# Optimization experiments

Measured on AMD Instinct MI355X. Metric: run time of the kernel, lower is better.

## Reference

```python
import jax, jax.numpy as jnp
import numpy as np

B, L, N_INP, N_HID = 128, 1000, 1, 1024
DT = 0.042
RHO = 0.99
INPUT_SCALING = 1.0
THETA_LIF = 1.0
THETA_RF = 1.0
LIF_TAU_M = 20.0
TAU_REF = 0.25
CONNECTIVITY = 0.1
GAMMA_RANGE = (2.7, 2.9)
EPS_RANGE = (4.7, 4.9)


def setup_inputs() -> dict:
    key = jax.random.key(0)
    x = jax.random.normal(key, (B, L, N_INP), dtype=jnp.float32)
    rng = np.random.default_rng(0)
    # per-unit oscillator params (tuple branch of __init__)
    gamma = rng.uniform(GAMMA_RANGE[0], GAMMA_RANGE[1], N_HID).astype(np.float32)
    epsilon = rng.uniform(EPS_RANGE[0], EPS_RANGE[1], N_HID).astype(np.float32)
    # recurrent matrix: uniform in [-2,2], rescaled to spectral norm rho
    h2h = rng.uniform(-2.0, 2.0, (N_HID, N_HID)).astype(np.float32)
    h2h = h2h * (RHO / np.linalg.norm(h2h, 2)).astype(np.float32)
    x2h = (rng.uniform(0.0, 1.0, (N_INP, N_HID)) * INPUT_SCALING).astype(np.float32)
    bias = ((rng.uniform(0.0, 1.0, N_HID) * 2.0 - 1.0) * INPUT_SCALING).astype(np.float32)
    mask = (rng.uniform(size=(N_HID, N_HID)) < CONNECTIVITY).astype(np.float32)
    lif2hrf = ((rng.uniform(0.0, 1.0, (N_HID, N_HID)) * 2.0 - 1.0) * 2.0 * mask).astype(np.float32)
    return {
        "x": x,
        "x2h": jnp.asarray(x2h),
        "h2h": jnp.asarray(h2h),
        "bias": jnp.asarray(bias),
        "lif2hrf": jnp.asarray(lif2hrf),
        "gamma": jnp.asarray(gamma),
        "epsilon": jnp.asarray(epsilon),
    }


def reference(x, x2h, h2h, bias, lif2hrf, gamma, epsilon):
    dtype = x.dtype
    Bv, Lv, _ = x.shape
    ref_decay = jnp.exp(jnp.asarray(-DT / TAU_REF, dtype))

    def step(carry, xt):
        hy, hz, lif_v, s, ref_p, hy_sum, hy_sq, hrf_n, lif_n = carry
        # input current: (B,I)@(I,H) + (B,H)@(H,H) + (H,)
        cur = xt @ x2h + s @ h2h + bias
        lif_v = lif_v + DT * (-lif_v / LIF_TAU_M + cur)
        lif_s = (lif_v > THETA_LIF).astype(dtype)
        lif_v = lif_v - lif_s * THETA_LIF
        drive = lif_s @ lif2hrf
        hz = hz + DT * (drive - gamma * hy - epsilon * hz)
        hy = hy + DT * hz
        s_new = (hy - THETA_RF - ref_p > 0).astype(dtype)
        # alpha = beta = 0 in bio_cell -> hy, hz unchanged by reset
        ref_p = ref_p * ref_decay + s_new
        hy_sum = hy_sum + hy
        hy_sq = hy_sq + hy * hy
        hrf_n = hrf_n + s_new.sum()
        lif_n = lif_n + lif_s.sum()
        return (hy, hz, lif_v, s_new, ref_p, hy_sum, hy_sq, hrf_n, lif_n), None

    z = jnp.zeros((Bv, N_HID), dtype)
    carry0 = (z, z, z, z, z, z, z, jnp.zeros((), dtype), jnp.zeros((), dtype))
    xs = jnp.swapaxes(x, 0, 1)  # (L, B, I)
    (hy, hz, lif_v, s, ref_p, hy_sum, hy_sq, hrf_n, lif_n), _ = jax.lax.scan(step, carry0, xs)

    hy_mean = hy_sum / Lv
    hy_rms = jnp.sqrt(hy_sq / Lv + 1e-8)
    hy_std = jnp.sqrt(jnp.clip(hy_sq / Lv - hy_mean ** 2, 1e-8))
    features = jnp.concatenate([hy_rms, hy_std, hy], axis=1)  # (B, 3*H)
    denom = Bv * Lv * N_HID
    r_hrf = hrf_n / denom
    r_lif = lif_n / denom
    r_total = r_hrf  # count_lif_spikes=False
    return features, r_total, r_hrf, r_lif
```

## Files before the change

kernel.cpp:

```cpp
#include <hip/hip_runtime.h>

#define NHID    1024
#define BATCH   128
#define LSTEPS  1000
#define DTC     0.042f
#define THETA   1.0f
#define TAUM    20.0f
#define LISTCAP 1032

__global__ __launch_bounds__(1024) void coesn_sim(
    const float* __restrict__ x,
    const float* __restrict__ x2h,
    const float* __restrict__ h2h,
    const float* __restrict__ bias,
    const float* __restrict__ lif2hrf,
    const float* __restrict__ gamma_,
    const float* __restrict__ eps_,
    float* __restrict__ out,
    unsigned int* __restrict__ ws)
{
    const int b    = blockIdx.x;
    const int h    = threadIdx.x;
    const int wv   = h >> 6;
    const int lane = h & 63;

    __shared__ unsigned int Ls[LISTCAP];
    __shared__ unsigned int Ll[LISTCAP];
    __shared__ int Cs[16], Cl[16];
    __shared__ unsigned int red[16];

    Ls[h] = 0; Ll[h] = 0;
    if (h < LISTCAP - 1024) { Ls[1024 + h] = 0; Ll[1024 + h] = 0; }
    if (h < 16) { Cs[h] = 0; Cl[h] = 0; }

    float hy = 0.f, hz = 0.f, v = 0.f, rp = 0.f;
    float hysum = 0.f, hysq = 0.f;
    unsigned int chrf = 0, clif = 0;

    const float g    = gamma_[h];
    const float e    = eps_[h];
    const float bi   = bias[h];
    const float win  = x2h[h];
    const float ref_decay = expf((float)(-0.042 / 0.25));
    const float* xb  = x + (size_t)b * LSTEPS;

    const char* hb = (const char*)h2h     + 4 * (size_t)h;
    const char* lb = (const char*)lif2hrf + 4 * (size_t)h;

    const unsigned long long below = (1ULL << lane) - 1ULL;

    int ns = 0;

    __syncthreads();

    for (int t = 0; t < LSTEPS; ++t) {
        const float xv = xb[t];
        float cur = xv * win + bi;
        for (int k = 0; k < ns; k += 8) {
            const unsigned o0 = Ls[k+0], o1 = Ls[k+1], o2 = Ls[k+2], o3 = Ls[k+3];
            const unsigned o4 = Ls[k+4], o5 = Ls[k+5], o6 = Ls[k+6], o7 = Ls[k+7];
            const float a0 = *(const float*)(hb + o0);
            const float a1 = *(const float*)(hb + o1);
            const float a2 = *(const float*)(hb + o2);
            const float a3 = *(const float*)(hb + o3);
            const float a4 = *(const float*)(hb + o4);
            const float a5 = *(const float*)(hb + o5);
            const float a6 = *(const float*)(hb + o6);
            const float a7 = *(const float*)(hb + o7);
            cur += a0;
            cur += (k+1 < ns) ? a1 : 0.0f;
            cur += (k+2 < ns) ? a2 : 0.0f;
            cur += (k+3 < ns) ? a3 : 0.0f;
            cur += (k+4 < ns) ? a4 : 0.0f;
            cur += (k+5 < ns) ? a5 : 0.0f;
            cur += (k+6 < ns) ? a6 : 0.0f;
            cur += (k+7 < ns) ? a7 : 0.0f;
        }

        v = v + DTC * (-v / TAUM + cur);
        const float lsp = (v > THETA) ? 1.f : 0.f;
        v -= lsp * THETA;
        clif += (unsigned)lsp;
        const unsigned long long balL = __ballot(lsp > 0.5f);
        if (lane == 0) Cl[wv] = __popcll(balL);
        __syncthreads();
        int pre = 0, nl = 0;
        for (int i = 0; i < 16; ++i) { const int c = Cl[i]; pre += (i < wv) ? c : 0; nl += c; }
        if (lsp > 0.5f) Ll[pre + __popcll(balL & below)] = (unsigned)(h * 4096);
        __syncthreads();

        float dr = 0.f;
        for (int k = 0; k < nl; k += 8) {
            const unsigned o0 = Ll[k+0], o1 = Ll[k+1], o2 = Ll[k+2], o3 = Ll[k+3];
            const unsigned o4 = Ll[k+4], o5 = Ll[k+5], o6 = Ll[k+6], o7 = Ll[k+7];
            const float a0 = *(const float*)(lb + o0);
            const float a1 = *(const float*)(lb + o1);
            const float a2 = *(const float*)(lb + o2);
            const float a3 = *(const float*)(lb + o3);
            const float a4 = *(const float*)(lb + o4);
            const float a5 = *(const float*)(lb + o5);
            const float a6 = *(const float*)(lb + o6);
            const float a7 = *(const float*)(lb + o7);
            dr += a0;
            dr += (k+1 < nl) ? a1 : 0.0f;
            dr += (k+2 < nl) ? a2 : 0.0f;
            dr += (k+3 < nl) ? a3 : 0.0f;
            dr += (k+4 < nl) ? a4 : 0.0f;
            dr += (k+5 < nl) ? a5 : 0.0f;
            dr += (k+6 < nl) ? a6 : 0.0f;
            dr += (k+7 < nl) ? a7 : 0.0f;
        }

        hz = hz + DTC * (dr - g * hy - e * hz);
        hy = hy + DTC * hz;
        const float sn = ((hy - THETA - rp) > 0.f) ? 1.f : 0.f;
        rp = rp * ref_decay + sn;
        hysum += hy;
        hysq  += hy * hy;
        chrf += (unsigned)sn;
        const unsigned long long balS = __ballot(sn > 0.5f);
        if (lane == 0) Cs[wv] = __popcll(balS);
        __syncthreads();
        pre = 0; ns = 0;
        for (int i = 0; i < 16; ++i) { const int c = Cs[i]; pre += (i < wv) ? c : 0; ns += c; }
        if (sn > 0.5f) Ls[pre + __popcll(balS & below)] = (unsigned)(h * 4096);
        __syncthreads();
    }

    const float Lf   = (float)LSTEPS;
    const float mean = hysum / Lf;
    const float rms  = sqrtf(hysq / Lf + 1e-8f);
    float var = hysq / Lf - mean * mean;
    var = fmaxf(var, 1e-8f);
    float* ob = out + (size_t)b * (3 * NHID);
    ob[h]            = rms;
    ob[NHID + h]     = sqrtf(var);
    ob[2 * NHID + h] = hy;

    unsigned int c = chrf;
    for (int off = 32; off > 0; off >>= 1) c += __shfl_down(c, off, 64);
    if (lane == 0) red[wv] = c;
    __syncthreads();
    if (h == 0) {
        unsigned int tot = 0;
        for (int i = 0; i < 16; ++i) tot += red[i];
        ws[b * 2] = tot;
    }
    __syncthreads();
    c = clif;
    for (int off = 32; off > 0; off >>= 1) c += __shfl_down(c, off, 64);
    if (lane == 0) red[wv] = c;
    __syncthreads();
    if (h == 0) {
        unsigned int tot = 0;
        for (int i = 0; i < 16; ++i) tot += red[i];
        ws[b * 2 + 1] = tot;
    }
}

__global__ void coesn_final(const unsigned int* __restrict__ ws,
                            float* __restrict__ out)
{
    if (threadIdx.x == 0 && blockIdx.x == 0) {
        unsigned long long hrf = 0, lif = 0;
        for (int b = 0; b < BATCH; ++b) {
            hrf += ws[b * 2];
            lif += ws[b * 2 + 1];
        }
        const float denom = (float)BATCH * (float)LSTEPS * (float)NHID;
        const float r_hrf = (float)hrf / denom;
        const float r_lif = (float)lif / denom;
        float* s = out + (size_t)BATCH * 3 * NHID;
        s[0] = r_hrf;
        s[1] = r_hrf;
        s[2] = r_lif;
    }
}

extern "C" void kernel_launch(void* const* d_in, const int* in_sizes, int n_in,
                              void* d_out, int out_size, void* d_ws, size_t ws_size,
                              hipStream_t stream) {
    const float* x       = (const float*)d_in[0];
    const float* x2h     = (const float*)d_in[1];
    const float* h2h     = (const float*)d_in[2];
    const float* bias    = (const float*)d_in[3];
    const float* lif2hrf = (const float*)d_in[4];
    const float* gamma_  = (const float*)d_in[5];
    const float* eps_    = (const float*)d_in[6];
    float* out = (float*)d_out;
    unsigned int* wsp = (unsigned int*)d_ws;

    coesn_sim<<<BATCH, NHID, 0, stream>>>(x, x2h, h2h, bias, lif2hrf, gamma_, eps_, out, wsp);
    coesn_final<<<1, 64, 0, stream>>>(wsp, out);
}
```

Measured before the change: 1.584 ms.

## Broadcast spike lists via readlane and software-pipeline sparse row gathers

Each wave now loads the first 256 spike-list entries from LDS into registers (one per lane) and uses readlane to turn each offset into a scalar. This replaces per-iteration LDS loads of list indices and makes row addresses wave-uniform. The gather loop is software-pipelined so the next 8 rows load while the previous 8 are accumulated. The wave-count prefix sum also switches from 16 LDS reads to one LDS read plus readlane broadcasts. Lists longer than 256 entries fall back to a slow scalar tail loop, and the padded list capacity is removed.

```diff
diff --git a/kernel.cpp b/kernel.cpp
--- a/kernel.cpp
+++ b/kernel.cpp
@@ -6,7 +6,53 @@
 #define DTC     0.042f
 #define THETA   1.0f
 #define TAUM    20.0f
-#define LISTCAP 1032
+
+#define RL(VS,I)  ((unsigned)__builtin_amdgcn_readlane((VS),(I)))
+
+__device__ __forceinline__ float gather_rows(float acc, const char* mat, int h,
+                                             const unsigned* __restrict__ Lds,
+                                             int v0, int v1, int v2, int v3, int n)
+{
+    if (n <= 0) return acc;
+    const int nf = (n < 256) ? n : 256;
+    const int M  = (nf + 7) & ~7;
+    float c0,c1,c2,c3,c4,c5,c6,c7;
+    {
+        const unsigned q0=RL(v0,0),q1=RL(v0,1),q2=RL(v0,2),q3=RL(v0,3),
+                       q4=RL(v0,4),q5=RL(v0,5),q6=RL(v0,6),q7=RL(v0,7);
+        c0=((const float*)(mat+q0))[h]; c1=((const float*)(mat+q1))[h];
+        c2=((const float*)(mat+q2))[h]; c3=((const float*)(mat+q3))[h];
+        c4=((const float*)(mat+q4))[h]; c5=((const float*)(mat+q5))[h];
+        c6=((const float*)(mat+q6))[h]; c7=((const float*)(mat+q7))[h];
+    }
+    int k = 8;
+    #pragma unroll 1
+    for (; k < M; k += 8) {
+        const int vs = (k < 64) ? v0 : (k < 128) ? v1 : (k < 192) ? v2 : v3;
+        const int kb = k & 63;
+        const unsigned t0=RL(vs,kb+0),t1=RL(vs,kb+1),t2=RL(vs,kb+2),t3=RL(vs,kb+3),
+                       t4=RL(vs,kb+4),t5=RL(vs,kb+5),t6=RL(vs,kb+6),t7=RL(vs,kb+7);
+        const float d0=((const float*)(mat+t0))[h], d1=((const float*)(mat+t1))[h],
+                    d2=((const float*)(mat+t2))[h], d3=((const float*)(mat+t3))[h],
+                    d4=((const float*)(mat+t4))[h], d5=((const float*)(mat+t5))[h],
+                    d6=((const float*)(mat+t6))[h], d7=((const float*)(mat+t7))[h];
+        acc += c0; acc += c1; acc += c2; acc += c3;
+        acc += c4; acc += c5; acc += c6; acc += c7;
+        c0=d0; c1=d1; c2=d2; c3=d3; c4=d4; c5=d5; c6=d6; c7=d7;
+    }
+    const int base = k - 8;
+    acc += c0;
+    acc += (base+1 < nf) ? c1 : 0.0f;
+    acc += (base+2 < nf) ? c2 : 0.0f;
+    acc += (base+3 < nf) ? c3 : 0.0f;
+    acc += (base+4 < nf) ? c4 : 0.0f;
+    acc += (base+5 < nf) ? c5 : 0.0f;
+    acc += (base+6 < nf) ? c6 : 0.0f;
+    acc += (base+7 < nf) ? c7 : 0.0f;
+    for (int kk = 256; kk < n; ++kk)
+        acc += ((const float*)(mat + Lds[kk]))[h];
+    return acc;
+}
 
 __global__ __launch_bounds__(1024) void coesn_sim(
     const float* __restrict__ x,
@@ -23,14 +69,14 @@
     const int h    = threadIdx.x;
     const int wv   = h >> 6;
     const int lane = h & 63;
-
-    __shared__ unsigned int Ls[LISTCAP];
-    __shared__ unsigned int Ll[LISTCAP];
+    const int wvs  = __builtin_amdgcn_readfirstlane(wv);
+
+    __shared__ unsigned int Ls[1024];
+    __shared__ unsigned int Ll[1024];
     __shared__ int Cs[16], Cl[16];
     __shared__ unsigned int red[16];
 
     Ls[h] = 0; Ll[h] = 0;
-    if (h < LISTCAP - 1024) { Ls[1024 + h] = 0; Ll[1024 + h] = 0; }
     if (h < 16) { Cs[h] = 0; Cl[h] = 0; }
 
     float hy = 0.f, hz = 0.f, v = 0.f, rp = 0.f;
@@ -44,8 +90,8 @@
     const float ref_decay = expf((float)(-0.042 / 0.25));
     const float* xb  = x + (size_t)b * LSTEPS;
 
-    const char* hb = (const char*)h2h     + 4 * (size_t)h;
-    const char* lb = (const char*)lif2hrf + 4 * (size_t)h;
+    const char* hmat = (const char*)h2h;
+    const char* lmat = (const char*)lif2hrf;
 
     const unsigned long long below = (1ULL << lane) - 1ULL;
 
@@ -54,62 +100,36 @@
     __syncthreads();
 
     for (int t = 0; t < LSTEPS; ++t) {
+        const int s0 = (int)Ls[lane];
+        const int s1 = (int)Ls[64 + lane];
+        const int s2 = (int)Ls[128 + lane];
+        const int s3 = (int)Ls[192 + lane];
         const float xv = xb[t];
-        float cur = xv * win + bi;
-        for (int k = 0; k < ns; k += 8) {
-            const unsigned o0 = Ls[k+0], o1 = Ls[k+1], o2 = Ls[k+2], o3 = Ls[k+3];
-            const unsigned o4 = Ls[k+4], o5 = Ls[k+5], o6 = Ls[k+6], o7 = Ls[k+7];
-            const float a0 = *(const float*)(hb + o0);
-            const float a1 = *(const float*)(hb + o1);
-            const float a2 = *(const float*)(hb + o2);
-            const float a3 = *(const float*)(hb + o3);
-            const float a4 = *(const float*)(hb + o4);
-            const float a5 = *(const float*)(hb + o5);
-            const float a6 = *(const float*)(hb + o6);
-            const float a7 = *(const float*)(hb + o7);
-            cur += a0;
-            cur += (k+1 < ns) ? a1 : 0.0f;
-            cur += (k+2 < ns) ? a2 : 0.0f;
-            cur += (k+3 < ns) ? a3 : 0.0f;
-            cur += (k+4 < ns) ? a4 : 0.0f;
-            cur += (k+5 < ns) ? a5 : 0.0f;
-            cur += (k+6 < ns) ? a6 : 0.0f;
-            cur += (k+7 < ns) ? a7 : 0.0f;
-        }
+        const float cur = gather_rows(xv * win + bi, hmat, h, Ls, s0, s1, s2, s3, ns);
 
         v = v + DTC * (-v / TAUM + cur);
         const float lsp = (v > THETA) ? 1.f : 0.f;
         v -= lsp * THETA;
         clif += (unsigned)lsp;
         const unsigned long long balL = __ballot(lsp > 0.5f);
-        if (lane == 0) Cl[wv] = __popcll(balL);
-        __syncthreads();
+        if (lane == 0) Cl[wv] = (int)__popcll(balL);
+        __syncthreads();
+        int cv = Cl[lane & 15];
         int pre = 0, nl = 0;
-        for (int i = 0; i < 16; ++i) { const int c = Cl[i]; pre += (i < wv) ? c : 0; nl += c; }
-        if (lsp > 0.5f) Ll[pre + __popcll(balL & below)] = (unsigned)(h * 4096);
-        __syncthreads();
-
-        float dr = 0.f;
-        for (int k = 0; k < nl; k += 8) {
-            const unsigned o0 = Ll[k+0], o1 = Ll[k+1], o2 = Ll[k+2], o3 = Ll[k+3];
-            const unsigned o4 = Ll[k+4], o5 = Ll[k+5], o6 = Ll[k+6], o7 = Ll[k+7];
-            const float a0 = *(const float*)(lb + o0);
-            const float a1 = *(const float*)(lb + o1);
-            const float a2 = *(const float*)(lb + o2);
-            const float a3 = *(const float*)(lb + o3);
-            const float a4 = *(const float*)(lb + o4);
-            const float a5 = *(const float*)(lb + o5);
-            const float a6 = *(const float*)(lb + o6);
-            const float a7 = *(const float*)(lb + o7);
-            dr += a0;
-            dr += (k+1 < nl) ? a1 : 0.0f;
-            dr += (k+2 < nl) ? a2 : 0.0f;
-            dr += (k+3 < nl) ? a3 : 0.0f;
-            dr += (k+4 < nl) ? a4 : 0.0f;
-            dr += (k+5 < nl) ? a5 : 0.0f;
-            dr += (k+6 < nl) ? a6 : 0.0f;
-            dr += (k+7 < nl) ? a7 : 0.0f;
+        #pragma unroll
+        for (int i = 0; i < 16; ++i) {
+            const int ci = __builtin_amdgcn_readlane(cv, i);
+            nl += ci;
+            pre += (i < wvs) ? ci : 0;
         }
+        if (lsp > 0.5f) Ll[pre + (int)__popcll(balL & below)] = (unsigned)(h * 4096);
+        __syncthreads();
+
+        const int l0 = (int)Ll[lane];
+        const int l1 = (int)Ll[64 + lane];
+        const int l2 = (int)Ll[128 + lane];
+        const int l3 = (int)Ll[192 + lane];
+        const float dr = gather_rows(0.0f, lmat, h, Ll, l0, l1, l2, l3, nl);
 
         hz = hz + DTC * (dr - g * hy - e * hz);
         hy = hy + DTC * hz;
@@ -119,11 +139,17 @@
         hysq  += hy * hy;
         chrf += (unsigned)sn;
         const unsigned long long balS = __ballot(sn > 0.5f);
-        if (lane == 0) Cs[wv] = __popcll(balS);
-        __syncthreads();
+        if (lane == 0) Cs[wv] = (int)__popcll(balS);
+        __syncthreads();
+        cv = Cs[lane & 15];
         pre = 0; ns = 0;
-        for (int i = 0; i < 16; ++i) { const int c = Cs[i]; pre += (i < wv) ? c : 0; ns += c; }
-        if (sn > 0.5f) Ls[pre + __popcll(balS & below)] = (unsigned)(h * 4096);
+        #pragma unroll
+        for (int i = 0; i < 16; ++i) {
+            const int ci = __builtin_amdgcn_readlane(cv, i);
+            ns += ci;
+            pre += (i < wvs) ? ci : 0;
+        }
+        if (sn > 0.5f) Ls[pre + (int)__popcll(balS & below)] = (unsigned)(h * 4096);
         __syncthreads();
     }
 
```

Result: slower. 1.868 ms (+17.9%).

## Compress sparse lif2hrf into bitmask+prefix rows for the spike-driven drive gather

Applied to the files above, without the earlier changes.

Adds a pre-pass kernel that packs each lif2hrf row into a 1 KB record: a per-32-column bitmask with prefix counts, followed by only the nonzero values. The simulation then gathers the drive term through this record, looking up each value with a popcount. Mask loads for the next group of eight spikes are software-prefetched ahead of use. The goal is to shrink the working set of the sparse matrix from 4 MB to about 1 MB so it stays cache-resident, at the cost of a dependent two-step load per spike. Rows with more than 192 nonzeros are silently truncated, so correctness relies on the roughly 10% connectivity. The compressed path runs only if the workspace is large enough.

```diff
diff --git a/kernel.cpp b/kernel.cpp
--- a/kernel.cpp
+++ b/kernel.cpp
@@ -7,7 +7,46 @@
 #define THETA   1.0f
 #define TAUM    20.0f
 #define LISTCAP 1032
-
+#define CMP_STRIDE 1024
+#define CMP_OFF    4096
+#define CMP_NEED   (CMP_OFF + (size_t)NHID * CMP_STRIDE + 64)
+
+__global__ __launch_bounds__(64) void build_cmp(const float* __restrict__ lif2hrf,
+                                                unsigned int* __restrict__ cmp)
+{
+    const int j = blockIdx.x;
+    const int l = threadIdx.x;
+    __shared__ float row[NHID];
+    __shared__ unsigned cnt[32];
+    const float* src = lif2hrf + (size_t)j * NHID;
+    for (int i = l; i < NHID; i += 64) row[i] = src[i];
+    __syncthreads();
+    unsigned int* dst = cmp + (size_t)j * (CMP_STRIDE / 4);
+    unsigned bits = 0, c = 0;
+    if (l < 32) {
+        #pragma unroll
+        for (int i = 0; i < 32; ++i)
+            if (row[l * 32 + i] != 0.0f) { bits |= (1u << i); ++c; }
+        cnt[l] = c;
+    }
+    __syncthreads();
+    if (l < 32) {
+        unsigned pre = 0;
+        for (int i = 0; i < 32; ++i) pre += ((unsigned)i < (unsigned)l) ? cnt[i] : 0;
+        dst[2 * l]     = bits;
+        dst[2 * l + 1] = pre;
+        unsigned idx = pre;
+        for (int i = 0; i < 32; ++i) {
+            const float v = row[l * 32 + i];
+            if (v != 0.0f) {
+                if (idx < 192) dst[64 + idx] = __float_as_uint(v);
+                ++idx;
+            }
+        }
+    }
+}
+
+template<bool CMPQ>
 __global__ __launch_bounds__(1024) void coesn_sim(
     const float* __restrict__ x,
     const float* __restrict__ x2h,
@@ -16,6 +55,7 @@
     const float* __restrict__ lif2hrf,
     const float* __restrict__ gamma_,
     const float* __restrict__ eps_,
+    const unsigned char* __restrict__ cmpb,
     float* __restrict__ out,
     unsigned int* __restrict__ ws)
 {
@@ -48,6 +88,9 @@
     const char* lb = (const char*)lif2hrf + 4 * (size_t)h;
 
     const unsigned long long below = (1ULL << lane) - 1ULL;
+    const unsigned mslot   = 8u * (unsigned)(h >> 5);
+    const unsigned bitm    = 1u << (h & 31);
+    const unsigned below32 = bitm - 1u;
 
     int ns = 0;
 
@@ -82,33 +125,76 @@
         v -= lsp * THETA;
         clif += (unsigned)lsp;
         const unsigned long long balL = __ballot(lsp > 0.5f);
-        if (lane == 0) Cl[wv] = __popcll(balL);
+        if (lane == 0) Cl[wv] = (int)__popcll(balL);
         __syncthreads();
         int pre = 0, nl = 0;
-        for (int i = 0; i < 16; ++i) { const int c = Cl[i]; pre += (i < wv) ? c : 0; nl += c; }
-        if (lsp > 0.5f) Ll[pre + __popcll(balL & below)] = (unsigned)(h * 4096);
+        #pragma unroll
+        for (int i = 0; i < 16; ++i) { const int ci = Cl[i]; nl += ci; pre += (i < wv) ? ci : 0; }
+        if (lsp > 0.5f)
+            Ll[pre + (int)__popcll(balL & below)] = (unsigned)(h * (CMPQ ? CMP_STRIDE : 4096));
         __syncthreads();
 
         float dr = 0.f;
-        for (int k = 0; k < nl; k += 8) {
-            const unsigned o0 = Ll[k+0], o1 = Ll[k+1], o2 = Ll[k+2], o3 = Ll[k+3];
-            const unsigned o4 = Ll[k+4], o5 = Ll[k+5], o6 = Ll[k+6], o7 = Ll[k+7];
-            const float a0 = *(const float*)(lb + o0);
-            const float a1 = *(const float*)(lb + o1);
-            const float a2 = *(const float*)(lb + o2);
-            const float a3 = *(const float*)(lb + o3);
-            const float a4 = *(const float*)(lb + o4);
-            const float a5 = *(const float*)(lb + o5);
-            const float a6 = *(const float*)(lb + o6);
-            const float a7 = *(const float*)(lb + o7);
-            dr += a0;
-            dr += (k+1 < nl) ? a1 : 0.0f;
-            dr += (k+2 < nl) ? a2 : 0.0f;
-            dr += (k+3 < nl) ? a3 : 0.0f;
-            dr += (k+4 < nl) ? a4 : 0.0f;
-            dr += (k+5 < nl) ? a5 : 0.0f;
-            dr += (k+6 < nl) ? a6 : 0.0f;
-            dr += (k+7 < nl) ? a7 : 0.0f;
+        if (CMPQ) {
+            if (nl > 0) {
+                unsigned off[8];
+                unsigned long long m[8];
+                #pragma unroll
+                for (int i = 0; i < 8; ++i) off[i] = Ll[i];
+                #pragma unroll
+                for (int i = 0; i < 8; ++i)
+                    m[i] = *(const unsigned long long*)(cmpb + off[i] + mslot);
+                for (int k = 0; k < nl; k += 8) {
+                    unsigned noff[8];
+                    unsigned long long nm[8];
+                    if (k + 8 < nl) {
+                        #pragma unroll
+                        for (int i = 0; i < 8; ++i) noff[i] = Ll[k + 8 + i];
+                        #pragma unroll
+                        for (int i = 0; i < 8; ++i)
+                            nm[i] = *(const unsigned long long*)(cmpb + noff[i] + mslot);
+                    } else {
+                        #pragma unroll
+                        for (int i = 0; i < 8; ++i) { noff[i] = off[i]; nm[i] = m[i]; }
+                    }
+                    float val[8];
+                    #pragma unroll
+                    for (int i = 0; i < 8; ++i) {
+                        const unsigned bits = (unsigned)m[i];
+                        const unsigned pfx  = (unsigned)(m[i] >> 32);
+                        const unsigned idx  = pfx + (unsigned)__popc(bits & below32);
+                        val[i] = *(const float*)(cmpb + off[i] + 256u + 4u * idx);
+                    }
+                    #pragma unroll
+                    for (int i = 0; i < 8; ++i) {
+                        const bool hit = ((unsigned)m[i] & bitm) != 0u;
+                        dr += ((k + i < nl) && hit) ? val[i] : 0.0f;
+                    }
+                    #pragma unroll
+                    for (int i = 0; i < 8; ++i) { off[i] = noff[i]; m[i] = nm[i]; }
+                }
+            }
+        } else {
+            for (int k = 0; k < nl; k += 8) {
+                const unsigned o0 = Ll[k+0], o1 = Ll[k+1], o2 = Ll[k+2], o3 = Ll[k+3];
+                const unsigned o4 = Ll[k+4], o5 = Ll[k+5], o6 = Ll[k+6], o7 = Ll[k+7];
+                const float a0 = *(const float*)(lb + o0);
+                const float a1 = *(const float*)(lb + o1);
+                const float a2 = *(const float*)(lb + o2);
+                const float a3 = *(const float*)(lb + o3);
+                const float a4 = *(const float*)(lb + o4);
+                const float a5 = *(const float*)(lb + o5);
+                const float a6 = *(const float*)(lb + o6);
+                const float a7 = *(const float*)(lb + o7);
+                dr += a0;
+                dr += (k+1 < nl) ? a1 : 0.0f;
+                dr += (k+2 < nl) ? a2 : 0.0f;
+                dr += (k+3 < nl) ? a3 : 0.0f;
+                dr += (k+4 < nl) ? a4 : 0.0f;
+                dr += (k+5 < nl) ? a5 : 0.0f;
+                dr += (k+6 < nl) ? a6 : 0.0f;
+                dr += (k+7 < nl) ? a7 : 0.0f;
+            }
         }
 
         hz = hz + DTC * (dr - g * hy - e * hz);
@@ -119,11 +205,12 @@
         hysq  += hy * hy;
         chrf += (unsigned)sn;
         const unsigned long long balS = __ballot(sn > 0.5f);
-        if (lane == 0) Cs[wv] = __popcll(balS);
+        if (lane == 0) Cs[wv] = (int)__popcll(balS);
         __syncthreads();
         pre = 0; ns = 0;
-        for (int i = 0; i < 16; ++i) { const int c = Cs[i]; pre += (i < wv) ? c : 0; ns += c; }
-        if (sn > 0.5f) Ls[pre + __popcll(balS & below)] = (unsigned)(h * 4096);
+        #pragma unroll
+        for (int i = 0; i < 16; ++i) { const int ci = Cs[i]; ns += ci; pre += (i < wv) ? ci : 0; }
+        if (sn > 0.5f) Ls[pre + (int)__popcll(balS & below)] = (unsigned)(h * 4096);
         __syncthreads();
     }
 
@@ -190,6 +277,15 @@
     float* out = (float*)d_out;
     unsigned int* wsp = (unsigned int*)d_ws;
 
-    coesn_sim<<<BATCH, NHID, 0, stream>>>(x, x2h, h2h, bias, lif2hrf, gamma_, eps_, out, wsp);
+    if (ws_size >= CMP_NEED) {
+        unsigned int* cmp = (unsigned int*)((char*)d_ws + CMP_OFF);
+        build_cmp<<<NHID, 64, 0, stream>>>(lif2hrf, cmp);
+        coesn_sim<true><<<BATCH, NHID, 0, stream>>>(x, x2h, h2h, bias, lif2hrf,
+                                                    gamma_, eps_,
+                                                    (const unsigned char*)cmp, out, wsp);
+    } else {
+        coesn_sim<false><<<BATCH, NHID, 0, stream>>>(x, x2h, h2h, bias, lif2hrf,
+                                                     gamma_, eps_, nullptr, out, wsp);
+    }
     coesn_final<<<1, 64, 0, stream>>>(wsp, out);
 }
```

Result: slower. 3.593 ms (+126.8%).
